# Kernel optimization log

Measured on AMD Instinct MI355X. Metric: run time of the kernel, lower is better.

## Reference

```python
import jax, jax.numpy as jnp
import numpy as np

UNITS = 400
FEAT = 3


def setup_inputs() -> dict:
    key = jax.random.key(0)
    ks = jax.random.split(key, 9)
    s_in = 1.0 / np.sqrt(FEAT)
    s_h = 1.0 / np.sqrt(UNITS)
    return {
        "inputs": jax.random.normal(ks[0], (64, 1000, FEAT), dtype=jnp.float32),
        "W_x": jax.random.normal(ks[1], (FEAT, 4 * UNITS), dtype=jnp.float32) * s_in,
        "W_h": jax.random.normal(ks[2], (UNITS, 4 * UNITS), dtype=jnp.float32) * s_h,
        "b": jnp.zeros((4 * UNITS,), dtype=jnp.float32),
        "p_i": jax.random.normal(ks[3], (UNITS,), dtype=jnp.float32) * 0.1,
        "p_f": jax.random.normal(ks[4], (UNITS,), dtype=jnp.float32) * 0.1,
        "p_o": jax.random.normal(ks[5], (UNITS,), dtype=jnp.float32) * 0.1,
        "W_out": jax.random.normal(ks[6], (UNITS, FEAT), dtype=jnp.float32) * s_h,
        "b_out": jnp.zeros((FEAT,), dtype=jnp.float32),
    }


def reference(inputs, W_x, W_h, b, p_i, p_f, p_o, W_out, b_out):
    B, T, _ = inputs.shape
    # Precompute input projections for all timesteps: [B, T, 4U]
    x_proj = jnp.einsum("btf,fg->btg", inputs, W_x) + b

    def step(carry, xp_t):
        h, c = carry  # [B, U] each
        z = xp_t + h @ W_h  # [B, 4U]
        zi, zf, zg, zo = jnp.split(z, 4, axis=-1)
        i = jax.nn.sigmoid(zi + p_i * c)  # peephole on c_prev
        f = jax.nn.sigmoid(zf + p_f * c)
        g = jnp.tanh(zg)
        c_new = f * c + i * g
        o = jax.nn.sigmoid(zo + p_o * c_new)  # peephole on new c
        h_new = o * jnp.tanh(c_new)
        return (h_new, c_new), h_new

    h0 = jnp.zeros((B, UNITS), dtype=inputs.dtype)
    c0 = jnp.zeros((B, UNITS), dtype=inputs.dtype)
    # scan over time: x_proj transposed to [T, B, 4U]
    _, hs = jax.lax.scan(step, (h0, c0), jnp.swapaxes(x_proj, 0, 1))
    hs = jnp.swapaxes(hs, 0, 1)  # [B, T, U]
    return jnp.einsum("btu,uf->btf", hs, W_out) + b_out
```

## Files before the change

kernel.cpp:

```cpp
#include <hip/hip_runtime.h>
#include <hip/hip_bf16.h>
#include <stdint.h>

#define UNITS 400
#define GATES 1600
#define TLEN  1000
#define BATCH 64

#define NBLK 16
#define NGRP 16
#define BPG  4
#define UPB  25
#define CPB  100
#define KK   20
#define KCH  20
#define FLAG_STRIDE 32

#define WBUF_OFF  0
#define WBUF_SZ   (NBLK*UNITS*CPB*4)
#define HBUF_OFF  (WBUF_OFF + WBUF_SZ)
#define HBUF_SZ   (2*BATCH*UNITS*4)
#define CTR_OFF   (HBUF_OFF + HBUF_SZ)
#define CTR_SZ    (NGRP*FLAG_STRIDE*4)
#define FLAGS_OFF (CTR_OFF + CTR_SZ)
#define FLAGS_SZ  (NGRP*NBLK*FLAG_STRIDE*4)
#define PART_OFF  (FLAGS_OFF + FLAGS_SZ)
#define PART_SZ   (NGRP*NBLK*BPG*3*TLEN*4)
#define WS_R4     ((size_t)FLAGS_OFF)
#define WS_FULL   ((size_t)PART_OFF + PART_SZ)

__device__ __forceinline__ float sigmoid_(float x) {
    return 1.0f / (1.0f + __expf(-x));
}
__device__ __forceinline__ float tanh_(float x) {
    return 1.0f - 2.0f / (__expf(2.0f * x) + 1.0f);
}

__global__ void reorder_w(const float* __restrict__ W_h, float* __restrict__ wbuf) {
    int i = blockIdx.x * 256 + threadIdx.x;
    if (i >= NBLK * UNITS * CPB) return;
    int c = i % CPB;
    int k = (i / CPB) % UNITS;
    int j = i / (CPB * UNITS);
    int g = c / UPB, u2 = c % UPB;
    int col = g * UNITS + j * UPB + u2;
    wbuf[i] = W_h[k * GATES + col];
}

template<int MODE>
__global__ __launch_bounds__(512, 1) void lstm_mb(
    const float* __restrict__ x,
    const float* __restrict__ W_x,
    const float* __restrict__ bvec,
    const float* __restrict__ p_i,
    const float* __restrict__ p_f,
    const float* __restrict__ p_o,
    const float* __restrict__ W_out,
    const float* __restrict__ b_out,
    const float* __restrict__ wbuf,
    float*       __restrict__ hbuf,
    unsigned int* __restrict__ ctr,
    unsigned int* __restrict__ flags,
    float*       __restrict__ part,
    float*       __restrict__ out)
{
    const int gr  = blockIdx.x % NGRP;
    const int j   = blockIdx.x / NGRP;
    const int tid = threadIdx.x;
    const int lane = tid & 63;
    const int wv   = tid >> 6;

    __shared__ float hsh[BPG][UNITS];
    __shared__ float zpart[KK][BPG][CPB];
    __shared__ float zsh[BPG][CPB];
    __shared__ float csh[BPG][UPB];
    __shared__ float xsh[BPG][4];
    __shared__ float red[8][4];
    __shared__ float wosh[UPB][3];

    const float* wslice = wbuf + (size_t)j * UNITS * CPB;

    const int kk = tid / 25, cq = tid % 25;
    const bool zrole = (tid < KK * 25);
    const int k0 = kk * KCH;
    const int rb = tid / CPB, rc = tid % CPB;
    const int gb = tid / UPB, gu = tid % UPB;

    float4 wreg[KCH];
    if (zrole) {
        #pragma unroll
        for (int r = 0; r < KCH; ++r)
            wreg[r] = *(const float4*)&wslice[(size_t)(k0 + r) * CPB + cq * 4];
    }

    float wx0 = 0.f, wx1 = 0.f, wx2 = 0.f, bbv = 0.f;
    if (tid < BPG * CPB) {
        int gcol = (rc / UPB) * UNITS + j * UPB + (rc % UPB);
        wx0 = W_x[0 * GATES + gcol];
        wx1 = W_x[1 * GATES + gcol];
        wx2 = W_x[2 * GATES + gcol];
        bbv = bvec[gcol];
    }
    float piu = 0.f, pfu = 0.f, pou = 0.f;
    int unit = 0;
    if (tid < BPG * UPB) {
        unit = j * UPB + gu;
        piu = p_i[unit]; pfu = p_f[unit]; pou = p_o[unit];
    }
    float wo0 = 0.f, wo1 = 0.f, wo2 = 0.f;
    if (MODE == 1 && tid < UNITS) {
        wo0 = W_out[tid * 3 + 0];
        wo1 = W_out[tid * 3 + 1];
        wo2 = W_out[tid * 3 + 2];
    }
    const float bo = (tid < 3) ? b_out[tid] : 0.f;
    if (MODE == 0 && tid < UPB * 3) {
        wosh[tid / 3][tid % 3] = W_out[(j * UPB + tid / 3) * 3 + (tid % 3)];
    }

    if (tid < UNITS) {
        #pragma unroll
        for (int b = 0; b < BPG; ++b) hsh[b][tid] = 0.f;
    }
    if (tid < BPG * UPB) csh[gb][gu] = 0.f;
    __syncthreads();

    unsigned int* myctr = ctr + gr * FLAG_STRIDE;

    for (int t = 0; t < TLEN; ++t) {
        const int p = t & 1;

        if (tid < BPG * 3) {
            int b = tid / 3, f = tid % 3;
            xsh[b][f] = x[((size_t)(gr * BPG + b) * TLEN + t) * 3 + f];
        }

        if (zrole) {
            float4 a0 = {0,0,0,0}, a1 = a0, a2 = a0, a3 = a0;
            #pragma unroll
            for (int ro = 0; ro < KCH; ro += 4) {
                const float4 h0 = *(const float4*)&hsh[0][k0 + ro];
                const float4 h1 = *(const float4*)&hsh[1][k0 + ro];
                const float4 h2 = *(const float4*)&hsh[2][k0 + ro];
                const float4 h3 = *(const float4*)&hsh[3][k0 + ro];
                #pragma unroll
                for (int dr = 0; dr < 4; ++dr) {
                    const float4 w = wreg[ro + dr];
                    const float e0 = (dr==0)?h0.x:(dr==1)?h0.y:(dr==2)?h0.z:h0.w;
                    const float e1 = (dr==0)?h1.x:(dr==1)?h1.y:(dr==2)?h1.z:h1.w;
                    const float e2 = (dr==0)?h2.x:(dr==1)?h2.y:(dr==2)?h2.z:h2.w;
                    const float e3 = (dr==0)?h3.x:(dr==1)?h3.y:(dr==2)?h3.z:h3.w;
                    a0.x = fmaf(e0, w.x, a0.x); a0.y = fmaf(e0, w.y, a0.y);
                    a0.z = fmaf(e0, w.z, a0.z); a0.w = fmaf(e0, w.w, a0.w);
                    a1.x = fmaf(e1, w.x, a1.x); a1.y = fmaf(e1, w.y, a1.y);
                    a1.z = fmaf(e1, w.z, a1.z); a1.w = fmaf(e1, w.w, a1.w);
                    a2.x = fmaf(e2, w.x, a2.x); a2.y = fmaf(e2, w.y, a2.y);
                    a2.z = fmaf(e2, w.z, a2.z); a2.w = fmaf(e2, w.w, a2.w);
                    a3.x = fmaf(e3, w.x, a3.x); a3.y = fmaf(e3, w.y, a3.y);
                    a3.z = fmaf(e3, w.z, a3.z); a3.w = fmaf(e3, w.w, a3.w);
                }
            }
            *(float4*)&zpart[kk][0][cq * 4] = a0;
            *(float4*)&zpart[kk][1][cq * 4] = a1;
            *(float4*)&zpart[kk][2][cq * 4] = a2;
            *(float4*)&zpart[kk][3][cq * 4] = a3;
        }
        __syncthreads();

        if (tid < BPG * CPB) {
            float s = fmaf(xsh[rb][0], wx0,
                      fmaf(xsh[rb][1], wx1,
                      fmaf(xsh[rb][2], wx2, bbv)));
            #pragma unroll
            for (int q = 0; q < KK; ++q) s += zpart[q][rb][rc];
            zsh[rb][rc] = s;
        }
        __syncthreads();

        if (tid < BPG * UPB) {
            const float cc = csh[gb][gu];
            const float zi = zsh[gb][gu];
            const float zf = zsh[gb][UPB   + gu];
            const float zg = zsh[gb][2*UPB + gu];
            const float zo = zsh[gb][3*UPB + gu];
            const float ig = sigmoid_(fmaf(piu, cc, zi));
            const float fg = sigmoid_(fmaf(pfu, cc, zf));
            const float gg = tanh_(zg);
            const float cn = fmaf(fg, cc, ig * gg);
            const float og = sigmoid_(fmaf(pou, cn, zo));
            const float hn = og * tanh_(cn);
            csh[gb][gu] = cn;
            if (MODE == 0) hsh[gb][unit] = hn;
            const int batch = gr * BPG + gb;
            __hip_atomic_store(&hbuf[(size_t)p * BATCH * UNITS + batch * UNITS + unit],
                               hn, __ATOMIC_RELAXED, __HIP_MEMORY_SCOPE_AGENT);
        }
        __syncthreads();

        if (MODE == 0) {
            if (tid == 0)
                __hip_atomic_store(&flags[(gr * NBLK + j) * FLAG_STRIDE],
                                   (unsigned)(t + 1),
                                   __ATOMIC_RELAXED, __HIP_MEMORY_SCOPE_AGENT);

            if (tid < BPG * 3) {
                const int pb = tid / 3, pf = tid % 3;
                float s = 0.f;
                #pragma unroll
                for (int u = 0; u < UPB; ++u)
                    s += hsh[pb][j * UPB + u] * wosh[u][pf];
                part[(((size_t)(gr * NBLK + j) * BPG + pb) * 3 + pf) * TLEN + t] = s;
            }

            {
                const unsigned target = (unsigned)(t + 1);
                for (;;) {
                    unsigned v = target;
                    if (lane < NBLK)
                        v = __hip_atomic_load(&flags[(gr * NBLK + lane) * FLAG_STRIDE],
                                              __ATOMIC_RELAXED, __HIP_MEMORY_SCOPE_AGENT);
                    if (__ballot(v < target) == 0ull) break;
                    __builtin_amdgcn_s_sleep(1);
                }
            }

            if (tid < UNITS) {
                #pragma unroll
                for (int b = 0; b < BPG; ++b)
                    hsh[b][tid] = __hip_atomic_load(
                        &hbuf[(size_t)p * BATCH * UNITS + (gr * BPG + b) * UNITS + tid],
                        __ATOMIC_RELAXED, __HIP_MEMORY_SCOPE_AGENT);
            }
            __syncthreads();
        } else {
            if (tid == 0) {
                __hip_atomic_fetch_add(myctr, 1u, __ATOMIC_RELAXED, __HIP_MEMORY_SCOPE_AGENT);
                const unsigned target = (unsigned)NBLK * (unsigned)(t + 1);
                while (__hip_atomic_load(myctr, __ATOMIC_RELAXED, __HIP_MEMORY_SCOPE_AGENT) < target) {
                    __builtin_amdgcn_s_sleep(1);
                }
            }
            __syncthreads();

            if (tid < UNITS) {
                #pragma unroll
                for (int b = 0; b < BPG; ++b)
                    hsh[b][tid] = __hip_atomic_load(
                        &hbuf[(size_t)p * BATCH * UNITS + (gr * BPG + b) * UNITS + tid],
                        __ATOMIC_RELAXED, __HIP_MEMORY_SCOPE_AGENT);
            }
            __syncthreads();

            if (j < BPG) {
                float s0 = 0.f, s1 = 0.f, s2 = 0.f;
                if (tid < UNITS) {
                    const float hv = hsh[j][tid];
                    s0 = hv * wo0; s1 = hv * wo1; s2 = hv * wo2;
                }
                #pragma unroll
                for (int off = 32; off; off >>= 1) {
                    s0 += __shfl_down(s0, off);
                    s1 += __shfl_down(s1, off);
                    s2 += __shfl_down(s2, off);
                }
                if (lane == 0) { red[wv][0] = s0; red[wv][1] = s1; red[wv][2] = s2; }
            }
            __syncthreads();
            if (j < BPG && tid < 3) {
                float r = bo;
                #pragma unroll
                for (int w2 = 0; w2 < 8; ++w2) r += red[w2][tid];
                out[((size_t)(gr * BPG + j) * TLEN + t) * 3 + tid] = r;
            }
        }
    }
}

__global__ void finish_y(const float* __restrict__ part,
                         const float* __restrict__ b_out,
                         float* __restrict__ out) {
    int i = blockIdx.x * 256 + threadIdx.x;
    if (i >= BATCH * TLEN * 3) return;
    const int f = i % 3;
    const int bt = i / 3;
    const int t = bt % TLEN;
    const int b = bt / TLEN;
    const int gr = b >> 2, gb = b & 3;
    float s = b_out[f];
    #pragma unroll
    for (int j = 0; j < NBLK; ++j)
        s += part[(((size_t)(gr * NBLK + j) * BPG + gb) * 3 + f) * TLEN + t];
    out[i] = s;
}

__global__ __launch_bounds__(512) void lstm_fused_fb(
    const float* __restrict__ x, const float* __restrict__ W_x,
    const float* __restrict__ W_h, const float* __restrict__ bvec,
    const float* __restrict__ p_i, const float* __restrict__ p_f,
    const float* __restrict__ p_o, const float* __restrict__ W_out,
    const float* __restrict__ b_out, float* __restrict__ out)
{
    const int b = blockIdx.x, tid = threadIdx.x;
    const int lane = tid & 63, wv = tid >> 6;
    __shared__ float hsh[UNITS], csh[UNITS], zsh[GATES], xb[3], red[8][3];
    const float4* Wh4 = (const float4*)W_h;
    const int g = tid;
    float4 wx0, wx1, wx2, bb;
    if (g < GATES/4) {
        const float4* Wx4 = (const float4*)W_x;
        wx0 = Wx4[0*400 + g]; wx1 = Wx4[1*400 + g]; wx2 = Wx4[2*400 + g];
        bb  = ((const float4*)bvec)[g];
    }
    float piu=0.f,pfu=0.f,pou=0.f,wo0=0.f,wo1=0.f,wo2=0.f;
    if (tid < UNITS) {
        piu=p_i[tid]; pfu=p_f[tid]; pou=p_o[tid];
        wo0=W_out[tid*3]; wo1=W_out[tid*3+1]; wo2=W_out[tid*3+2];
        hsh[tid]=0.f; csh[tid]=0.f;
    }
    const float bo = (tid<3)?b_out[tid]:0.f;
    const float* xrow = x + (size_t)b*TLEN*3;
    float* orow = out + (size_t)b*TLEN*3;
    for (int t=0;t<TLEN;++t){
        if (tid<3) xb[tid]=xrow[t*3+tid];
        __syncthreads();
        const float x0=xb[0],x1=xb[1],x2=xb[2];
        if (g < GATES/4){
            float4 acc;
            acc.x=fmaf(x0,wx0.x,fmaf(x1,wx1.x,fmaf(x2,wx2.x,bb.x)));
            acc.y=fmaf(x0,wx0.y,fmaf(x1,wx1.y,fmaf(x2,wx2.y,bb.y)));
            acc.z=fmaf(x0,wx0.z,fmaf(x1,wx1.z,fmaf(x2,wx2.z,bb.z)));
            acc.w=fmaf(x0,wx0.w,fmaf(x1,wx1.w,fmaf(x2,wx2.w,bb.w)));
            const float4* wp=Wh4+g;
            #pragma unroll 8
            for(int k=0;k<UNITS;++k){
                const float hk=hsh[k]; const float4 w=wp[(size_t)k*400];
                acc.x=fmaf(hk,w.x,acc.x); acc.y=fmaf(hk,w.y,acc.y);
                acc.z=fmaf(hk,w.z,acc.z); acc.w=fmaf(hk,w.w,acc.w);
            }
            ((float4*)zsh)[g]=acc;
        }
        __syncthreads();
        float s0=0.f,s1=0.f,s2=0.f;
        if (tid<UNITS){
            const float cc=csh[tid];
            const float zi=zsh[tid],zf=zsh[tid+UNITS],zg=zsh[tid+2*UNITS],zo=zsh[tid+3*UNITS];
            const float ig=sigmoid_(fmaf(piu,cc,zi));
            const float fg=sigmoid_(fmaf(pfu,cc,zf));
            const float gg=tanh_(zg);
            const float cn=fmaf(fg,cc,ig*gg);
            const float og=sigmoid_(fmaf(pou,cn,zo));
            const float hn=og*tanh_(cn);
            csh[tid]=cn; hsh[tid]=hn;
            s0=hn*wo0; s1=hn*wo1; s2=hn*wo2;
        }
        #pragma unroll
        for(int off=32;off;off>>=1){
            s0+=__shfl_down(s0,off); s1+=__shfl_down(s1,off); s2+=__shfl_down(s2,off);
        }
        if(lane==0){red[wv][0]=s0;red[wv][1]=s1;red[wv][2]=s2;}
        __syncthreads();
        if(tid<3){
            float r=bo;
            #pragma unroll
            for(int w2=0;w2<8;++w2) r+=red[w2][tid];
            orow[t*3+tid]=r;
        }
    }
}

extern "C" void kernel_launch(void* const* d_in, const int* in_sizes, int n_in,
                              void* d_out, int out_size, void* d_ws, size_t ws_size,
                              hipStream_t stream) {
    const float* x     = (const float*)d_in[0];
    const float* W_x   = (const float*)d_in[1];
    const float* W_h   = (const float*)d_in[2];
    const float* b     = (const float*)d_in[3];
    const float* p_i   = (const float*)d_in[4];
    const float* p_f   = (const float*)d_in[5];
    const float* p_o   = (const float*)d_in[6];
    const float* W_out = (const float*)d_in[7];
    const float* b_out = (const float*)d_in[8];
    float* out = (float*)d_out;

    if (ws_size < WS_R4) {
        lstm_fused_fb<<<BATCH, 512, 0, stream>>>(x, W_x, W_h, b, p_i, p_f, p_o,
                                                 W_out, b_out, out);
        return;
    }

    uint8_t* ws = (uint8_t*)d_ws;
    float* wbuf = (float*)(ws + WBUF_OFF);
    float* hbuf = (float*)(ws + HBUF_OFF);
    unsigned int* ctr   = (unsigned int*)(ws + CTR_OFF);
    unsigned int* flags = (unsigned int*)(ws + FLAGS_OFF);
    float* part = (float*)(ws + PART_OFF);

    reorder_w<<<(NBLK * UNITS * CPB + 255) / 256, 256, 0, stream>>>(W_h, wbuf);

    if (ws_size >= WS_FULL) {
        hipMemsetAsync(flags, 0, FLAGS_SZ, stream);
        lstm_mb<0><<<NGRP * NBLK, 512, 0, stream>>>(x, W_x, b, p_i, p_f, p_o,
                                                    W_out, b_out, wbuf, hbuf,
                                                    ctr, flags, part, out);
        finish_y<<<(BATCH * TLEN * 3 + 255) / 256, 256, 0, stream>>>(part, b_out, out);
    } else {
        hipMemsetAsync(ctr, 0, CTR_SZ, stream);
        lstm_mb<1><<<NGRP * NBLK, 512, 0, stream>>>(x, W_x, b, p_i, p_f, p_o,
                                                    W_out, b_out, wbuf, hbuf,
                                                    ctr, flags, part, out);
    }
}
```

Before: 3.565 ms.

## Pack timestep tag with hidden value to replace flag-based inter-block sync

```diff
diff --git a/kernel.cpp b/kernel.cpp
--- a/kernel.cpp
+++ b/kernel.cpp
@@ -19,14 +19,12 @@
 #define WBUF_OFF  0
 #define WBUF_SZ   (NBLK*UNITS*CPB*4)
 #define HBUF_OFF  (WBUF_OFF + WBUF_SZ)
-#define HBUF_SZ   (2*BATCH*UNITS*4)
+#define HBUF_SZ   (2*BATCH*UNITS*8)
 #define CTR_OFF   (HBUF_OFF + HBUF_SZ)
 #define CTR_SZ    (NGRP*FLAG_STRIDE*4)
-#define FLAGS_OFF (CTR_OFF + CTR_SZ)
-#define FLAGS_SZ  (NGRP*NBLK*FLAG_STRIDE*4)
-#define PART_OFF  (FLAGS_OFF + FLAGS_SZ)
+#define PART_OFF  (CTR_OFF + CTR_SZ)
 #define PART_SZ   (NGRP*NBLK*BPG*3*TLEN*4)
-#define WS_R4     ((size_t)FLAGS_OFF)
+#define WS_R4     ((size_t)PART_OFF)
 #define WS_FULL   ((size_t)PART_OFF + PART_SZ)
 
 __device__ __forceinline__ float sigmoid_(float x) {
@@ -58,9 +56,9 @@
     const float* __restrict__ W_out,
     const float* __restrict__ b_out,
     const float* __restrict__ wbuf,
-    float*       __restrict__ hbuf,
+    unsigned long long* __restrict__ hbuf64,
+    float*       __restrict__ hbuf32,
     unsigned int* __restrict__ ctr,
-    unsigned int* __restrict__ flags,
     float*       __restrict__ part,
     float*       __restrict__ out)
 {
@@ -190,19 +188,22 @@
             const float og = sigmoid_(fmaf(pou, cn, zo));
             const float hn = og * tanh_(cn);
             csh[gb][gu] = cn;
-            if (MODE == 0) hsh[gb][unit] = hn;
             const int batch = gr * BPG + gb;
-            __hip_atomic_store(&hbuf[(size_t)p * BATCH * UNITS + batch * UNITS + unit],
-                               hn, __ATOMIC_RELAXED, __HIP_MEMORY_SCOPE_AGENT);
+            if (MODE == 0) {
+                hsh[gb][unit] = hn;
+                const unsigned long long pkt =
+                    ((unsigned long long)(unsigned)(t + 1) << 32) |
+                    (unsigned long long)__float_as_uint(hn);
+                __hip_atomic_store(&hbuf64[(size_t)p * BATCH * UNITS + batch * UNITS + unit],
+                                   pkt, __ATOMIC_RELAXED, __HIP_MEMORY_SCOPE_AGENT);
+            } else {
+                __hip_atomic_store(&hbuf32[(size_t)p * BATCH * UNITS + batch * UNITS + unit],
+                                   hn, __ATOMIC_RELAXED, __HIP_MEMORY_SCOPE_AGENT);
+            }
         }
         __syncthreads();
 
         if (MODE == 0) {
-            if (tid == 0)
-                __hip_atomic_store(&flags[(gr * NBLK + j) * FLAG_STRIDE],
-                                   (unsigned)(t + 1),
-                                   __ATOMIC_RELAXED, __HIP_MEMORY_SCOPE_AGENT);
-
             if (tid < BPG * 3) {
                 const int pb = tid / 3, pf = tid % 3;
                 float s = 0.f;
@@ -212,24 +213,29 @@
                 part[(((size_t)(gr * NBLK + j) * BPG + pb) * 3 + pf) * TLEN + t] = s;
             }
 
-            {
-                const unsigned target = (unsigned)(t + 1);
+            if (tid < UNITS) {
+                const unsigned want = (unsigned)(t + 1);
+                const size_t base = (size_t)p * BATCH * UNITS
+                                  + (size_t)gr * BPG * UNITS + tid;
+                unsigned long long v0, v1, v2, v3;
                 for (;;) {
-                    unsigned v = target;
-                    if (lane < NBLK)
-                        v = __hip_atomic_load(&flags[(gr * NBLK + lane) * FLAG_STRIDE],
-                                              __ATOMIC_RELAXED, __HIP_MEMORY_SCOPE_AGENT);
-                    if (__ballot(v < target) == 0ull) break;
+                    v0 = __hip_atomic_load(&hbuf64[base + 0 * UNITS],
+                                           __ATOMIC_RELAXED, __HIP_MEMORY_SCOPE_AGENT);
+                    v1 = __hip_atomic_load(&hbuf64[base + 1 * UNITS],
+                                           __ATOMIC_RELAXED, __HIP_MEMORY_SCOPE_AGENT);
+                    v2 = __hip_atomic_load(&hbuf64[base + 2 * UNITS],
+                                           __ATOMIC_RELAXED, __HIP_MEMORY_SCOPE_AGENT);
+                    v3 = __hip_atomic_load(&hbuf64[base + 3 * UNITS],
+                                           __ATOMIC_RELAXED, __HIP_MEMORY_SCOPE_AGENT);
+                    if ((unsigned)(v0 >> 32) == want && (unsigned)(v1 >> 32) == want &&
+                        (unsigned)(v2 >> 32) == want && (unsigned)(v3 >> 32) == want)
+                        break;
                     __builtin_amdgcn_s_sleep(1);
                 }
-            }
-
-            if (tid < UNITS) {
-                #pragma unroll
-                for (int b = 0; b < BPG; ++b)
-                    hsh[b][tid] = __hip_atomic_load(
-                        &hbuf[(size_t)p * BATCH * UNITS + (gr * BPG + b) * UNITS + tid],
-                        __ATOMIC_RELAXED, __HIP_MEMORY_SCOPE_AGENT);
+                hsh[0][tid] = __uint_as_float((unsigned)v0);
+                hsh[1][tid] = __uint_as_float((unsigned)v1);
+                hsh[2][tid] = __uint_as_float((unsigned)v2);
+                hsh[3][tid] = __uint_as_float((unsigned)v3);
             }
             __syncthreads();
         } else {
@@ -246,7 +252,7 @@
                 #pragma unroll
                 for (int b = 0; b < BPG; ++b)
                     hsh[b][tid] = __hip_atomic_load(
-                        &hbuf[(size_t)p * BATCH * UNITS + (gr * BPG + b) * UNITS + tid],
+                        &hbuf32[(size_t)p * BATCH * UNITS + (gr * BPG + b) * UNITS + tid],
                         __ATOMIC_RELAXED, __HIP_MEMORY_SCOPE_AGENT);
             }
             __syncthreads();
@@ -390,23 +396,23 @@
 
     uint8_t* ws = (uint8_t*)d_ws;
     float* wbuf = (float*)(ws + WBUF_OFF);
-    float* hbuf = (float*)(ws + HBUF_OFF);
-    unsigned int* ctr   = (unsigned int*)(ws + CTR_OFF);
-    unsigned int* flags = (unsigned int*)(ws + FLAGS_OFF);
+    unsigned long long* hbuf64 = (unsigned long long*)(ws + HBUF_OFF);
+    float* hbuf32 = (float*)(ws + HBUF_OFF);
+    unsigned int* ctr = (unsigned int*)(ws + CTR_OFF);
     float* part = (float*)(ws + PART_OFF);
 
     reorder_w<<<(NBLK * UNITS * CPB + 255) / 256, 256, 0, stream>>>(W_h, wbuf);
 
     if (ws_size >= WS_FULL) {
-        hipMemsetAsync(flags, 0, FLAGS_SZ, stream);
+        hipMemsetAsync(hbuf64, 0, HBUF_SZ, stream);
         lstm_mb<0><<<NGRP * NBLK, 512, 0, stream>>>(x, W_x, b, p_i, p_f, p_o,
-                                                    W_out, b_out, wbuf, hbuf,
-                                                    ctr, flags, part, out);
+                                                    W_out, b_out, wbuf,
+                                                    hbuf64, hbuf32, ctr, part, out);
         finish_y<<<(BATCH * TLEN * 3 + 255) / 256, 256, 0, stream>>>(part, b_out, out);
     } else {
         hipMemsetAsync(ctr, 0, CTR_SZ, stream);
         lstm_mb<1><<<NGRP * NBLK, 512, 0, stream>>>(x, W_x, b, p_i, p_f, p_o,
-                                                    W_out, b_out, wbuf, hbuf,
-                                                    ctr, flags, part, out);
-    }
-}
+                                                    W_out, b_out, wbuf,
+                                                    hbuf64, hbuf32, ctr, part, out);
+    }
+}
```

Measured after the change: 3.083 ms. 1.16x faster.
